# Kernel tuning notes

Measured on AMD Instinct MI355X. Metric: run time of the kernel, lower is better.

The kernel has to match this reference:

```python
import jax, jax.numpy as jnp
import numpy as np

# ---- config (from DAREConfig init_kwargs) ----
TAU = 0.1
RHO_VIS = 0.5          # is_visual=True -> rho_target = rho_vis_target
PREFIX_KAPPA = 64
LAMBDA_RATIO = 1.0
LAMBDA_SOFT = 0.1
LAMBDA_HARD = 1.0

B, S = 256, 32768


def setup_inputs() -> dict:
    key = jax.random.key(0)
    k1, k2 = jax.random.split(key)
    importance = jax.random.normal(k1, (B, S), dtype=jnp.float32)
    modality_mask = jax.random.randint(k2, (B, S), 0, 2) > 0  # bool [B,S]
    return {"importance": importance, "modality_mask": modality_mask}


def reference(importance, modality_mask):
    """Vectorized DAREController.route(is_visual=True, training=True).

    The torch loop over batch with data-dependent k is replaced by a
    per-row k-th-largest threshold: for each row, k_b = min(int(rho*|mm_b|),
    |valid_b|); tokens with score >= k_b-th largest valid score are kept
    (this matches DifferentiableTopK's hard mask soft>0.5, i.e. exactly the
    top-k scores, assuming no ties).
    """
    mm = modality_mask.astype(bool)          # [B,S]
    b, s = importance.shape

    target = jnp.clip(mm.sum(axis=1).astype(jnp.float32) * RHO_VIS, 1.0)  # [B]
    prefix = jnp.arange(s) < min(PREFIX_KAPPA, s)                          # [S]
    eff = mm & ~prefix[None, :]                                            # [B,S] routable tokens
    n_valid = eff.sum(axis=1)                                              # [B]
    k = jnp.minimum(target.astype(jnp.int32), n_valid)                     # [B] per-row top-k size

    neg_inf = jnp.float32(-jnp.inf)
    masked = jnp.where(eff, importance, neg_inf)                           # [B,S]
    sorted_desc = -jnp.sort(-masked, axis=1)                               # [B,S]
    idx = jnp.clip(k - 1, 0, s - 1)                                        # [B]
    thresh = jnp.take_along_axis(sorted_desc, idx[:, None], axis=1)        # [B,1]
    hard = masked >= thresh                                                # top-k of valid tokens

    keep_mask = prefix[None, :] | (hard & (k > 0)[:, None])                # [B,S]

    # ---- training / is_visual losses ----
    kept = (keep_mask & mm).sum(axis=1).astype(jnp.float32)
    denom = mm.sum(axis=1).astype(jnp.float32) + 1e-6
    actual_ratio = kept / denom
    loss_ratio = jnp.mean(jnp.abs(actual_ratio - RHO_VIS))                 # F.l1_loss

    dropped = mm & ~keep_mask
    n_drop = dropped.sum()
    drop_mean = jnp.sum(jnp.where(dropped, importance, 0.0)) / jnp.maximum(n_drop, 1).astype(jnp.float32)
    loss_soft = jnp.where(n_drop > 0, drop_mean, 0.0)

    loss_hard = jnp.mean(jnp.clip(RHO_VIS - actual_ratio, 0.0))

    return (keep_mask,
            LAMBDA_RATIO * loss_ratio,
            LAMBDA_SOFT * loss_soft,
            LAMBDA_HARD * loss_hard)
```

## Files before the change

### kernel.cpp

```cpp
#include <hip/hip_runtime.h>


#define NB 256
#define NS 32768
#define KAPPA 64
#define NT 1024
#define NCPY 64
#define HP 257
#define V4 (NS / NT / 4)

typedef float f32x4 __attribute__((ext_vector_type(4)));
typedef int   i32x4 __attribute__((ext_vector_type(4)));

__device__ __forceinline__ unsigned int fkey(float f) {
    unsigned int u = __float_as_uint(f);
    return (u & 0x80000000u) ? ~u : (u | 0x80000000u);
}

__device__ __forceinline__ float unkey(unsigned int k) {
    unsigned int u = (k & 0x80000000u) ? (k ^ 0x80000000u) : ~k;
    return __uint_as_float(u);
}

__global__ __launch_bounds__(NT) void dare_rows(const float* __restrict__ imp,
                                                const int* __restrict__ mask,
                                                float* __restrict__ keep,
                                                float* __restrict__ stats) {
    __shared__ unsigned int hist0[NCPY * HP];
    __shared__ unsigned int hist[256];
    __shared__ unsigned int wtot[4];
    __shared__ unsigned int sh_mm, sh_eff;
    __shared__ unsigned int sh_pref;
    __shared__ unsigned int sh_rem;
    __shared__ unsigned int sh_kept, sh_ndrop;
    __shared__ float sh_dsum;

    const int row = blockIdx.x;
    const int tid = threadIdx.x;
    const int lane = tid & 63;
    const int wid = tid >> 6;
    const f32x4* rimp4  = (const f32x4*)(imp  + (size_t)row * NS);
    const i32x4* rmask4 = (const i32x4*)(mask + (size_t)row * NS);
    f32x4*       rkeep4 = (f32x4*)      (keep + (size_t)row * NS);

    for (int i = tid; i < NCPY * HP; i += NT) hist0[i] = 0;
    if (tid < 256) hist[tid] = 0;
    if (tid == 0) {
        sh_mm = 0; sh_eff = 0; sh_kept = 0; sh_ndrop = 0; sh_dsum = 0.0f;
        sh_pref = 0; sh_rem = 1;
    }
    __syncthreads();

    unsigned int keys[V4 * 4];
    unsigned int effbits = 0, mmbits = 0;

    #pragma unroll
    for (int i = 0; i < V4; i++) {
        const int idx4 = tid + i * NT;
        const f32x4 v = rimp4[idx4];
        const i32x4 m = rmask4[idx4];
        #pragma unroll
        for (int j = 0; j < 4; j++) {
            const int e = i * 4 + j;
            const int col = idx4 * 4 + j;
            keys[e] = fkey(v[j]);
            const bool mm  = (m[j] != 0);
            const bool eff = mm && (col >= KAPPA);
            mmbits  |= (mm  ? 1u : 0u) << e;
            effbits |= (eff ? 1u : 0u) << e;
        }
    }

    unsigned int* myhist = &hist0[((wid << 2) | (lane & 3)) * HP];
    #pragma unroll
    for (int e = 0; e < V4 * 4; e++) {
        if ((effbits >> e) & 1u) atomicAdd(&myhist[keys[e] >> 24], 1u);
    }

    int mm_local  = __popc(mmbits);
    int eff_local = __popc(effbits);
    #pragma unroll
    for (int off = 32; off; off >>= 1) {
        mm_local  += __shfl_down(mm_local, off);
        eff_local += __shfl_down(eff_local, off);
    }
    if (lane == 0) {
        atomicAdd(&sh_mm,  (unsigned int)mm_local);
        atomicAdd(&sh_eff, (unsigned int)eff_local);
    }
    __syncthreads();

    #pragma unroll
    for (int pass = 0; pass < 4; pass++) {
        const int shift = 24 - 8 * pass;

        if (pass > 0) {
            if (tid < 256) hist[tid] = 0;
            __syncthreads();
            const unsigned int pmask = 0xFFFFFFFFu << (shift + 8);
            const unsigned int pref = sh_pref;
            #pragma unroll
            for (int e = 0; e < V4 * 4; e++) {
                const bool match = ((effbits >> e) & 1u) && ((keys[e] & pmask) == pref);
                if (match) atomicAdd(&hist[(keys[e] >> shift) & 0xFFu], 1u);
            }
            __syncthreads();
        }

        unsigned int h = 0, s = 0;
        if (tid < 256) {
            if (pass == 0) {
                #pragma unroll
                for (int c = 0; c < NCPY; c++) h += hist0[c * HP + tid];
            } else {
                h = hist[tid];
            }
            s = h;
            #pragma unroll
            for (int off = 1; off < 64; off <<= 1) {
                const unsigned int t = __shfl_down(s, off);
                if (lane + off < 64) s += t;
            }
            if (lane == 0) wtot[tid >> 6] = s;
        }
        __syncthreads();
        if (tid < 256) {
            unsigned int sfull = s;
            for (int w = (tid >> 6) + 1; w < 4; w++) sfull += wtot[w];
            unsigned int rem;
            if (pass == 0) {
                const float target = fmaxf((float)sh_mm * 0.5f, 1.0f);
                const int k = min((int)target, (int)sh_eff);
                rem = (unsigned int)max(k, 1);
            } else {
                rem = sh_rem;
            }
            if (sfull >= rem && (sfull - h) < rem) {
                sh_pref = (pass == 0) ? ((unsigned int)tid << 24)
                                      : (sh_pref | ((unsigned int)tid << shift));
                sh_rem = rem - (sfull - h);
            }
        }
        __syncthreads();
    }

    const unsigned int thresh = sh_pref;
    const float targetf = fmaxf((float)sh_mm * 0.5f, 1.0f);
    const bool kpos = (min((int)targetf, (int)sh_eff) > 0);

    int kept_l = 0, ndrop_l = 0;
    float dsum_l = 0.0f;
    #pragma unroll
    for (int i = 0; i < V4; i++) {
        const int idx4 = tid + i * NT;
        f32x4 o;
        #pragma unroll
        for (int j = 0; j < 4; j++) {
            const int e = i * 4 + j;
            const int col = idx4 * 4 + j;
            const bool mm  = (mmbits >> e) & 1u;
            const bool eff = (effbits >> e) & 1u;
            const bool hard = eff && kpos && (keys[e] >= thresh);
            const bool kp = (col < KAPPA) || hard;
            o[j] = kp ? 1.0f : 0.0f;
            kept_l += (kp && mm) ? 1 : 0;
            const bool drop = mm && !kp;
            ndrop_l += drop ? 1 : 0;
            dsum_l += drop ? unkey(keys[e]) : 0.0f;
        }
        rkeep4[idx4] = o;
    }
    #pragma unroll
    for (int off = 32; off; off >>= 1) {
        kept_l  += __shfl_down(kept_l, off);
        ndrop_l += __shfl_down(ndrop_l, off);
        dsum_l  += __shfl_down(dsum_l, off);
    }
    if (lane == 0) {
        atomicAdd(&sh_kept,  (unsigned int)kept_l);
        atomicAdd(&sh_ndrop, (unsigned int)ndrop_l);
        atomicAdd(&sh_dsum,  dsum_l);
    }
    __syncthreads();
    if (tid == 0) {
        stats[row * 4 + 0] = (float)sh_kept;
        stats[row * 4 + 1] = (float)sh_mm;
        stats[row * 4 + 2] = (float)sh_ndrop;
        stats[row * 4 + 3] = sh_dsum;
    }
}

__global__ __launch_bounds__(256) void dare_losses(const float* __restrict__ stats,
                                                   float* __restrict__ out) {
    __shared__ float w_a[4], w_h[4], w_n[4], w_d[4];
    const int tid = threadIdx.x;
    const float kept = stats[tid * 4 + 0];
    const float mmc  = stats[tid * 4 + 1];
    const float nd   = stats[tid * 4 + 2];
    const float ds   = stats[tid * 4 + 3];
    const float ratio = kept / (mmc + 1e-6f);
    float a = fabsf(ratio - 0.5f);
    float h = fmaxf(0.5f - ratio, 0.0f);
    float n = nd, d = ds;
    #pragma unroll
    for (int off = 32; off; off >>= 1) {
        a += __shfl_down(a, off);
        h += __shfl_down(h, off);
        n += __shfl_down(n, off);
        d += __shfl_down(d, off);
    }
    const int wid = tid >> 6, lane = tid & 63;
    if (lane == 0) { w_a[wid] = a; w_h[wid] = h; w_n[wid] = n; w_d[wid] = d; }
    __syncthreads();
    if (tid == 0) {
        float sa = 0.f, shh = 0.f, sn = 0.f, sd = 0.f;
        for (int w = 0; w < 4; w++) { sa += w_a[w]; shh += w_h[w]; sn += w_n[w]; sd += w_d[w]; }
        out[0] = sa / (float)NB;
        out[1] = (sn > 0.0f) ? 0.1f * (sd / fmaxf(sn, 1.0f)) : 0.0f;
        out[2] = shh / (float)NB;
    }
}

extern "C" void kernel_launch(void* const* d_in, const int* in_sizes, int n_in,
                              void* d_out, int out_size, void* d_ws, size_t ws_size,
                              hipStream_t stream) {
    const float* imp  = (const float*)d_in[0];
    const int*   mask = (const int*)d_in[1];
    float* out   = (float*)d_out;
    float* stats = (float*)d_ws;

    dare_rows<<<NB, NT, 0, stream>>>(imp, mask, out, stats);
    dare_losses<<<1, 256, 0, stream>>>(stats, out + (size_t)NB * NS);
}
```

Baseline: 112.4 us.

## Split row kernel into select pass and separate parallel mask-write pass

The single per-row kernel is split in two. A select kernel computes the radix-select threshold and packs the modality mask into a shared bitmap written to workspace. A second kernel launched with 8x more blocks then re-reads importance, applies the threshold, writes the keep mask and accumulates stats with global atomics. The histogram copies are also cut from 64 per block to one per wave. The split is meant to spread the output-write phase across more CUs and shrink shared memory, at the cost of re-reading importance, an extra launch and more bank conflicts in the histogram.

New measurement: 118.9 us. +5.8%, slower.

```diff
diff --git a/kernel.cpp b/kernel.cpp
--- a/kernel.cpp
+++ b/kernel.cpp
@@ -5,35 +5,36 @@
 #define NS 32768
 #define KAPPA 64
 #define NT 1024
-#define NCPY 64
+#define NW (NT / 64)
 #define HP 257
 #define V4 (NS / NT / 4)
 
+#define K2B 256
+#define K2SPLIT 8
+#define K2V4 (NS / K2SPLIT / K2B / 4)
+
 typedef float f32x4 __attribute__((ext_vector_type(4)));
 typedef int   i32x4 __attribute__((ext_vector_type(4)));
+
+#define WS_THRESH (4096 / 4)
+#define WS_KPOS   (5120 / 4)
+#define WS_BM     (8192 / 4)
 
 __device__ __forceinline__ unsigned int fkey(float f) {
     unsigned int u = __float_as_uint(f);
     return (u & 0x80000000u) ? ~u : (u | 0x80000000u);
 }
 
-__device__ __forceinline__ float unkey(unsigned int k) {
-    unsigned int u = (k & 0x80000000u) ? (k ^ 0x80000000u) : ~k;
-    return __uint_as_float(u);
-}
-
-__global__ __launch_bounds__(NT) void dare_rows(const float* __restrict__ imp,
-                                                const int* __restrict__ mask,
-                                                float* __restrict__ keep,
-                                                float* __restrict__ stats) {
-    __shared__ unsigned int hist0[NCPY * HP];
+__global__ __launch_bounds__(NT) void dare_select(const float* __restrict__ imp,
+                                                  const int* __restrict__ mask,
+                                                  unsigned int* __restrict__ ws) {
+    __shared__ unsigned int hist0[NW * HP];
     __shared__ unsigned int hist[256];
+    __shared__ unsigned int bm[NS / 32];
     __shared__ unsigned int wtot[4];
     __shared__ unsigned int sh_mm, sh_eff;
     __shared__ unsigned int sh_pref;
     __shared__ unsigned int sh_rem;
-    __shared__ unsigned int sh_kept, sh_ndrop;
-    __shared__ float sh_dsum;
 
     const int row = blockIdx.x;
     const int tid = threadIdx.x;
@@ -41,14 +42,11 @@
     const int wid = tid >> 6;
     const f32x4* rimp4  = (const f32x4*)(imp  + (size_t)row * NS);
     const i32x4* rmask4 = (const i32x4*)(mask + (size_t)row * NS);
-    f32x4*       rkeep4 = (f32x4*)      (keep + (size_t)row * NS);
-
-    for (int i = tid; i < NCPY * HP; i += NT) hist0[i] = 0;
+
+    for (int i = tid; i < NW * HP; i += NT) hist0[i] = 0;
     if (tid < 256) hist[tid] = 0;
-    if (tid == 0) {
-        sh_mm = 0; sh_eff = 0; sh_kept = 0; sh_ndrop = 0; sh_dsum = 0.0f;
-        sh_pref = 0; sh_rem = 1;
-    }
+    bm[tid] = 0;
+    if (tid == 0) { sh_mm = 0; sh_eff = 0; sh_pref = 0; sh_rem = 1; }
     __syncthreads();
 
     unsigned int keys[V4 * 4];
@@ -71,10 +69,16 @@
         }
     }
 
-    unsigned int* myhist = &hist0[((wid << 2) | (lane & 3)) * HP];
+    unsigned int* myhist = &hist0[wid * HP];
     #pragma unroll
     for (int e = 0; e < V4 * 4; e++) {
         if ((effbits >> e) & 1u) atomicAdd(&myhist[keys[e] >> 24], 1u);
+    }
+    #pragma unroll
+    for (int i = 0; i < V4; i++) {
+        const int idx4 = tid + i * NT;
+        const unsigned int nib = (mmbits >> (i * 4)) & 0xFu;
+        atomicOr(&bm[idx4 >> 3], nib << ((idx4 & 7) * 4));
     }
 
     int mm_local  = __popc(mmbits);
@@ -111,7 +115,7 @@
         if (tid < 256) {
             if (pass == 0) {
                 #pragma unroll
-                for (int c = 0; c < NCPY; c++) h += hist0[c * HP + tid];
+                for (int c = 0; c < NW; c++) h += hist0[c * HP + tid];
             } else {
                 h = hist[tid];
             }
@@ -144,49 +148,78 @@
         __syncthreads();
     }
 
-    const unsigned int thresh = sh_pref;
-    const float targetf = fmaxf((float)sh_mm * 0.5f, 1.0f);
-    const bool kpos = (min((int)targetf, (int)sh_eff) > 0);
+    ws[WS_BM + row * (NS / 32) + tid] = bm[tid];
+    if (tid == 0) {
+        const float target = fmaxf((float)sh_mm * 0.5f, 1.0f);
+        const int k = min((int)target, (int)sh_eff);
+        ws[WS_THRESH + row] = sh_pref;
+        ws[WS_KPOS + row] = (k > 0) ? 1u : 0u;
+        float* stats = (float*)ws;
+        stats[row * 4 + 0] = 0.0f;
+        stats[row * 4 + 1] = (float)sh_mm;
+        stats[row * 4 + 2] = 0.0f;
+        stats[row * 4 + 3] = 0.0f;
+    }
+}
+
+__global__ __launch_bounds__(K2B) void dare_write(const float* __restrict__ imp,
+                                                  const unsigned int* __restrict__ ws,
+                                                  float* __restrict__ keep) {
+    __shared__ float w_k[4], w_n[4], w_d[4];
+
+    const int row = blockIdx.x >> 3;
+    const int q   = blockIdx.x & 7;
+    const int tid = threadIdx.x;
+    const int lane = tid & 63;
+
+    const unsigned int thresh = ws[WS_THRESH + row];
+    const bool kpos = ws[WS_KPOS + row] != 0u;
+    const unsigned int* rbm = ws + WS_BM + row * (NS / 32);
+
+    const f32x4* rimp4  = (const f32x4*)(imp  + (size_t)row * NS);
+    f32x4*       rkeep4 = (f32x4*)      (keep + (size_t)row * NS);
 
     int kept_l = 0, ndrop_l = 0;
     float dsum_l = 0.0f;
-    #pragma unroll
-    for (int i = 0; i < V4; i++) {
-        const int idx4 = tid + i * NT;
+
+    #pragma unroll
+    for (int i = 0; i < K2V4; i++) {
+        const int idx4 = q * (NS / K2SPLIT / 4) + tid + i * K2B;
+        const f32x4 v = rimp4[idx4];
+        const unsigned int nib = (rbm[idx4 >> 3] >> ((idx4 & 7) * 4)) & 0xFu;
         f32x4 o;
         #pragma unroll
         for (int j = 0; j < 4; j++) {
-            const int e = i * 4 + j;
             const int col = idx4 * 4 + j;
-            const bool mm  = (mmbits >> e) & 1u;
-            const bool eff = (effbits >> e) & 1u;
-            const bool hard = eff && kpos && (keys[e] >= thresh);
+            const bool mm  = (nib >> j) & 1u;
+            const bool eff = mm && (col >= KAPPA);
+            const bool hard = eff && kpos && (fkey(v[j]) >= thresh);
             const bool kp = (col < KAPPA) || hard;
             o[j] = kp ? 1.0f : 0.0f;
             kept_l += (kp && mm) ? 1 : 0;
             const bool drop = mm && !kp;
             ndrop_l += drop ? 1 : 0;
-            dsum_l += drop ? unkey(keys[e]) : 0.0f;
+            dsum_l += drop ? v[j] : 0.0f;
         }
         rkeep4[idx4] = o;
     }
+
     #pragma unroll
     for (int off = 32; off; off >>= 1) {
         kept_l  += __shfl_down(kept_l, off);
         ndrop_l += __shfl_down(ndrop_l, off);
         dsum_l  += __shfl_down(dsum_l, off);
     }
-    if (lane == 0) {
-        atomicAdd(&sh_kept,  (unsigned int)kept_l);
-        atomicAdd(&sh_ndrop, (unsigned int)ndrop_l);
-        atomicAdd(&sh_dsum,  dsum_l);
-    }
+    const int wid = tid >> 6;
+    if (lane == 0) { w_k[wid] = (float)kept_l; w_n[wid] = (float)ndrop_l; w_d[wid] = dsum_l; }
     __syncthreads();
     if (tid == 0) {
-        stats[row * 4 + 0] = (float)sh_kept;
-        stats[row * 4 + 1] = (float)sh_mm;
-        stats[row * 4 + 2] = (float)sh_ndrop;
-        stats[row * 4 + 3] = sh_dsum;
+        float sk = 0.f, sn = 0.f, sd = 0.f;
+        for (int w = 0; w < 4; w++) { sk += w_k[w]; sn += w_n[w]; sd += w_d[w]; }
+        float* stats = (float*)ws;
+        atomicAdd(&stats[row * 4 + 0], sk);
+        atomicAdd(&stats[row * 4 + 2], sn);
+        atomicAdd(&stats[row * 4 + 3], sd);
     }
 }
 
@@ -226,9 +259,10 @@
                               hipStream_t stream) {
     const float* imp  = (const float*)d_in[0];
     const int*   mask = (const int*)d_in[1];
-    float* out   = (float*)d_out;
-    float* stats = (float*)d_ws;
-
-    dare_rows<<<NB, NT, 0, stream>>>(imp, mask, out, stats);
-    dare_losses<<<1, 256, 0, stream>>>(stats, out + (size_t)NB * NS);
-}
+    float* out = (float*)d_out;
+    unsigned int* ws = (unsigned int*)d_ws;
+
+    dare_select<<<NB, NT, 0, stream>>>(imp, mask, ws);
+    dare_write<<<NB * K2SPLIT, K2B, 0, stream>>>(imp, ws, out);
+    dare_losses<<<1, 256, 0, stream>>>((const float*)ws, out + (size_t)NB * NS);
+}
```

## Replace 4-pass radix select with 2048-bin histogram plus candidate bitwise select

Applied to the files above, without the earlier changes.

Swaps the four-pass 8-bit radix select for a single 11-bit histogram pass (one shared 2048-bin histogram instead of 64 padded copies). The elements that land in the threshold bin are compacted into shared memory, and one wavefront resolves the remaining 21 bits with ballot-based bitwise selection. Outputs that are clearly above or below the threshold bin are written right away; only vectors containing candidates are deferred until the exact threshold is known. The aim is to cut the three extra full-row histogram passes and their barriers. The cost is more atomic contention on the single histogram, a large shared candidate buffer that lowers occupancy, and a serial 21-bit loop run by only 64 threads.

New measurement: 111.3 us. About the same (-1.0%).

```diff
diff --git a/kernel.cpp b/kernel.cpp
--- a/kernel.cpp
+++ b/kernel.cpp
@@ -5,9 +5,10 @@
 #define NS 32768
 #define KAPPA 64
 #define NT 1024
-#define NCPY 64
-#define HP 257
 #define V4 (NS / NT / 4)
+#define NBIN 2048
+#define NSEG 256
+#define SEGW (NBIN / NSEG)
 
 typedef float f32x4 __attribute__((ext_vector_type(4)));
 typedef int   i32x4 __attribute__((ext_vector_type(4)));
@@ -26,12 +27,11 @@
                                                 const int* __restrict__ mask,
                                                 float* __restrict__ keep,
                                                 float* __restrict__ stats) {
-    __shared__ unsigned int hist0[NCPY * HP];
-    __shared__ unsigned int hist[256];
+    __shared__ unsigned int hist[NBIN];
+    __shared__ unsigned int cand[NS];
     __shared__ unsigned int wtot[4];
-    __shared__ unsigned int sh_mm, sh_eff;
-    __shared__ unsigned int sh_pref;
-    __shared__ unsigned int sh_rem;
+    __shared__ unsigned int sh_mm, sh_eff, sh_cand;
+    __shared__ unsigned int sh_b0, sh_rem, sh_thresh;
     __shared__ unsigned int sh_kept, sh_ndrop;
     __shared__ float sh_dsum;
 
@@ -43,11 +43,12 @@
     const i32x4* rmask4 = (const i32x4*)(mask + (size_t)row * NS);
     f32x4*       rkeep4 = (f32x4*)      (keep + (size_t)row * NS);
 
-    for (int i = tid; i < NCPY * HP; i += NT) hist0[i] = 0;
-    if (tid < 256) hist[tid] = 0;
+    hist[tid] = 0;
+    hist[tid + NT] = 0;
     if (tid == 0) {
-        sh_mm = 0; sh_eff = 0; sh_kept = 0; sh_ndrop = 0; sh_dsum = 0.0f;
-        sh_pref = 0; sh_rem = 1;
+        sh_mm = 0; sh_eff = 0; sh_cand = 0;
+        sh_b0 = 0; sh_rem = 1; sh_thresh = 0;
+        sh_kept = 0; sh_ndrop = 0; sh_dsum = 0.0f;
     }
     __syncthreads();
 
@@ -71,10 +72,9 @@
         }
     }
 
-    unsigned int* myhist = &hist0[((wid << 2) | (lane & 3)) * HP];
     #pragma unroll
     for (int e = 0; e < V4 * 4; e++) {
-        if ((effbits >> e) & 1u) atomicAdd(&myhist[keys[e] >> 24], 1u);
+        if ((effbits >> e) & 1u) atomicAdd(&hist[keys[e] >> 21], 1u);
     }
 
     int mm_local  = __popc(mmbits);
@@ -90,86 +90,142 @@
     }
     __syncthreads();
 
-    #pragma unroll
-    for (int pass = 0; pass < 4; pass++) {
-        const int shift = 24 - 8 * pass;
-
-        if (pass > 0) {
-            if (tid < 256) hist[tid] = 0;
-            __syncthreads();
-            const unsigned int pmask = 0xFFFFFFFFu << (shift + 8);
-            const unsigned int pref = sh_pref;
-            #pragma unroll
-            for (int e = 0; e < V4 * 4; e++) {
-                const bool match = ((effbits >> e) & 1u) && ((keys[e] & pmask) == pref);
-                if (match) atomicAdd(&hist[(keys[e] >> shift) & 0xFFu], 1u);
-            }
-            __syncthreads();
-        }
-
-        unsigned int h = 0, s = 0;
-        if (tid < 256) {
-            if (pass == 0) {
-                #pragma unroll
-                for (int c = 0; c < NCPY; c++) h += hist0[c * HP + tid];
-            } else {
-                h = hist[tid];
-            }
-            s = h;
-            #pragma unroll
-            for (int off = 1; off < 64; off <<= 1) {
-                const unsigned int t = __shfl_down(s, off);
-                if (lane + off < 64) s += t;
-            }
-            if (lane == 0) wtot[tid >> 6] = s;
-        }
-        __syncthreads();
-        if (tid < 256) {
-            unsigned int sfull = s;
-            for (int w = (tid >> 6) + 1; w < 4; w++) sfull += wtot[w];
-            unsigned int rem;
-            if (pass == 0) {
-                const float target = fmaxf((float)sh_mm * 0.5f, 1.0f);
-                const int k = min((int)target, (int)sh_eff);
-                rem = (unsigned int)max(k, 1);
-            } else {
-                rem = sh_rem;
-            }
-            if (sfull >= rem && (sfull - h) < rem) {
-                sh_pref = (pass == 0) ? ((unsigned int)tid << 24)
-                                      : (sh_pref | ((unsigned int)tid << shift));
-                sh_rem = rem - (sfull - h);
-            }
-        }
-        __syncthreads();
-    }
-
-    const unsigned int thresh = sh_pref;
-    const float targetf = fmaxf((float)sh_mm * 0.5f, 1.0f);
-    const bool kpos = (min((int)targetf, (int)sh_eff) > 0);
+    unsigned int r[SEGW];
+    unsigned int hsum = 0, s = 0;
+    if (tid < NSEG) {
+        #pragma unroll
+        for (int b = 0; b < SEGW; b++) { r[b] = hist[tid * SEGW + b]; hsum += r[b]; }
+        s = hsum;
+        #pragma unroll
+        for (int off = 1; off < 64; off <<= 1) {
+            const unsigned int t = __shfl_down(s, off);
+            if (lane + off < 64) s += t;
+        }
+        if (lane == 0) wtot[tid >> 6] = s;
+    }
+    __syncthreads();
+    if (tid < NSEG) {
+        unsigned int sfull = s;
+        for (int w = (tid >> 6) + 1; w < 4; w++) sfull += wtot[w];
+        const float target = fmaxf((float)sh_mm * 0.5f, 1.0f);
+        const int k = min((int)target, (int)sh_eff);
+        const unsigned int rem = (unsigned int)max(k, 1);
+        const unsigned int above = sfull - hsum;
+        if (sfull >= rem && above < rem) {
+            unsigned int cum = above;
+            #pragma unroll
+            for (int b = SEGW - 1; b >= 0; b--) {
+                if (cum + r[b] >= rem) { sh_b0 = tid * SEGW + b; sh_rem = rem - cum; break; }
+                cum += r[b];
+            }
+        }
+    }
+    __syncthreads();
+
+    const unsigned int b0 = sh_b0;
+    const bool kpos = (sh_eff > 0);
 
     int kept_l = 0, ndrop_l = 0;
     float dsum_l = 0.0f;
+    unsigned int defer = 0;
+
     #pragma unroll
     for (int i = 0; i < V4; i++) {
         const int idx4 = tid + i * NT;
-        f32x4 o;
+        unsigned int cm = 0;
         #pragma unroll
         for (int j = 0; j < 4; j++) {
             const int e = i * 4 + j;
-            const int col = idx4 * 4 + j;
-            const bool mm  = (mmbits >> e) & 1u;
             const bool eff = (effbits >> e) & 1u;
-            const bool hard = eff && kpos && (keys[e] >= thresh);
-            const bool kp = (col < KAPPA) || hard;
-            o[j] = kp ? 1.0f : 0.0f;
-            kept_l += (kp && mm) ? 1 : 0;
-            const bool drop = mm && !kp;
-            ndrop_l += drop ? 1 : 0;
-            dsum_l += drop ? unkey(keys[e]) : 0.0f;
-        }
-        rkeep4[idx4] = o;
-    }
+            const bool is_cand = kpos && eff && ((keys[e] >> 21) == b0);
+            cm |= (is_cand ? 1u : 0u) << j;
+        }
+        if (cm) {
+            defer |= 1u << i;
+            #pragma unroll
+            for (int j = 0; j < 4; j++) {
+                if ((cm >> j) & 1u) {
+                    const unsigned int pos = atomicAdd(&sh_cand, 1u);
+                    cand[pos] = keys[i * 4 + j];
+                }
+            }
+        } else {
+            f32x4 o;
+            #pragma unroll
+            for (int j = 0; j < 4; j++) {
+                const int e = i * 4 + j;
+                const int col = idx4 * 4 + j;
+                const bool mm  = (mmbits >> e) & 1u;
+                const bool eff = (effbits >> e) & 1u;
+                const bool hard = kpos && eff && ((keys[e] >> 21) > b0);
+                const bool kp = (col < KAPPA) || hard;
+                o[j] = kp ? 1.0f : 0.0f;
+                kept_l += (kp && mm) ? 1 : 0;
+                const bool drop = mm && !kp;
+                ndrop_l += drop ? 1 : 0;
+                dsum_l += drop ? unkey(keys[e]) : 0.0f;
+            }
+            rkeep4[idx4] = o;
+        }
+    }
+    __syncthreads();
+
+    if (tid < 64) {
+        const unsigned int cnt = sh_cand;
+        if (cnt > 0) {
+            unsigned int rem = sh_rem;
+            unsigned int pref = 0;
+            const int slots = (int)((cnt + 63u) >> 6);
+            unsigned int lowreg[16];
+            #pragma unroll
+            for (int sl = 0; sl < 16; sl++) {
+                const unsigned int idx = (unsigned int)lane + ((unsigned int)sl << 6);
+                lowreg[sl] = (idx < cnt) ? (cand[idx] & 0x1FFFFFu) : 0xFFFFFFFFu;
+            }
+            for (int bit = 20; bit >= 0; bit--) {
+                const unsigned int hi = pref >> (bit + 1);
+                unsigned int cnt1 = 0;
+                for (int sl = 0; sl < slots; sl++) {
+                    unsigned int lw;
+                    if (sl < 16) lw = lowreg[sl];
+                    else {
+                        const unsigned int idx = (unsigned int)lane + ((unsigned int)sl << 6);
+                        lw = (idx < cnt) ? (cand[idx] & 0x1FFFFFu) : 0xFFFFFFFFu;
+                    }
+                    const bool m = (lw >> (bit + 1)) == hi && ((lw >> bit) & 1u);
+                    cnt1 += (unsigned int)__popcll(__ballot(m));
+                }
+                if (cnt1 >= rem) pref |= 1u << bit; else rem -= cnt1;
+            }
+            if (lane == 0) sh_thresh = (b0 << 21) | pref;
+        }
+    }
+    __syncthreads();
+
+    const unsigned int thresh = sh_thresh;
+    #pragma unroll
+    for (int i = 0; i < V4; i++) {
+        if ((defer >> i) & 1u) {
+            const int idx4 = tid + i * NT;
+            f32x4 o;
+            #pragma unroll
+            for (int j = 0; j < 4; j++) {
+                const int e = i * 4 + j;
+                const int col = idx4 * 4 + j;
+                const bool mm  = (mmbits >> e) & 1u;
+                const bool eff = (effbits >> e) & 1u;
+                const bool hard = kpos && eff && (keys[e] >= thresh);
+                const bool kp = (col < KAPPA) || hard;
+                o[j] = kp ? 1.0f : 0.0f;
+                kept_l += (kp && mm) ? 1 : 0;
+                const bool drop = mm && !kp;
+                ndrop_l += drop ? 1 : 0;
+                dsum_l += drop ? unkey(keys[e]) : 0.0f;
+            }
+            rkeep4[idx4] = o;
+        }
+    }
+
     #pragma unroll
     for (int off = 32; off; off >>= 1) {
         kept_l  += __shfl_down(kept_l, off);
```

## Stage importance row in LDS via direct global-to-LDS loads, single shared histogram

Applied to the files above, without the earlier changes.

The importance row is now loaded straight into a 128KB LDS buffer with global_load_lds and re-read from LDS in every radix pass, so keys no longer sit in registers. The 64 privatized first-pass histogram copies are dropped in favour of one shared 256-bin histogram, and the mm/eff counts use per-wave slots instead of atomics. This cuts register pressure and histogram init/merge work, at the cost of repeated LDS reads and more atomic contention on the single histogram. The 128KB LDS footprint also limits residency to one block per CU.

Result: slower. 118.8 us (+5.7%).

```diff
diff --git a/kernel.cpp b/kernel.cpp
--- a/kernel.cpp
+++ b/kernel.cpp
@@ -5,34 +5,28 @@
 #define NS 32768
 #define KAPPA 64
 #define NT 1024
-#define NCPY 64
-#define HP 257
+#define NW (NT / 64)
 #define V4 (NS / NT / 4)
 
 typedef float f32x4 __attribute__((ext_vector_type(4)));
 typedef int   i32x4 __attribute__((ext_vector_type(4)));
-
-__device__ __forceinline__ unsigned int fkey(float f) {
-    unsigned int u = __float_as_uint(f);
+typedef unsigned int u32;
+
+__device__ __forceinline__ u32 fkey(float f) {
+    u32 u = __float_as_uint(f);
     return (u & 0x80000000u) ? ~u : (u | 0x80000000u);
-}
-
-__device__ __forceinline__ float unkey(unsigned int k) {
-    unsigned int u = (k & 0x80000000u) ? (k ^ 0x80000000u) : ~k;
-    return __uint_as_float(u);
 }
 
 __global__ __launch_bounds__(NT) void dare_rows(const float* __restrict__ imp,
                                                 const int* __restrict__ mask,
                                                 float* __restrict__ keep,
                                                 float* __restrict__ stats) {
-    __shared__ unsigned int hist0[NCPY * HP];
-    __shared__ unsigned int hist[256];
-    __shared__ unsigned int wtot[4];
-    __shared__ unsigned int sh_mm, sh_eff;
-    __shared__ unsigned int sh_pref;
-    __shared__ unsigned int sh_rem;
-    __shared__ unsigned int sh_kept, sh_ndrop;
+    __shared__ float simp[NS];
+    __shared__ u32 hist[256];
+    __shared__ u32 wtot[4];
+    __shared__ u32 wred_mm[NW], wred_eff[NW];
+    __shared__ u32 sh_mm, sh_eff, sh_pref, sh_rem;
+    __shared__ u32 sh_kept, sh_ndrop;
     __shared__ float sh_dsum;
 
     const int row = blockIdx.x;
@@ -43,40 +37,36 @@
     const i32x4* rmask4 = (const i32x4*)(mask + (size_t)row * NS);
     f32x4*       rkeep4 = (f32x4*)      (keep + (size_t)row * NS);
 
-    for (int i = tid; i < NCPY * HP; i += NT) hist0[i] = 0;
     if (tid < 256) hist[tid] = 0;
-    if (tid == 0) {
-        sh_mm = 0; sh_eff = 0; sh_kept = 0; sh_ndrop = 0; sh_dsum = 0.0f;
-        sh_pref = 0; sh_rem = 1;
-    }
-    __syncthreads();
-
-    unsigned int keys[V4 * 4];
-    unsigned int effbits = 0, mmbits = 0;
-
-    #pragma unroll
-    for (int i = 0; i < V4; i++) {
-        const int idx4 = tid + i * NT;
-        const f32x4 v = rimp4[idx4];
-        const i32x4 m = rmask4[idx4];
+    if (tid == 0) { sh_pref = 0; sh_rem = 1; sh_kept = 0; sh_ndrop = 0; sh_dsum = 0.0f; }
+
+    #pragma unroll
+    for (int i = 0; i < V4; i++) {
+        const int idx4 = tid + i * NT;
+        __builtin_amdgcn_global_load_lds(
+            (const __attribute__((address_space(1))) u32*)(&rimp4[idx4]),
+            (__attribute__((address_space(3))) u32*)(&simp[idx4 * 4]),
+            16, 0, 0);
+    }
+
+    i32x4 mv[V4];
+    #pragma unroll
+    for (int i = 0; i < V4; i++) mv[i] = rmask4[tid + i * NT];
+
+    u32 mmbits = 0, effbits = 0;
+    #pragma unroll
+    for (int i = 0; i < V4; i++) {
+        const int idx4 = tid + i * NT;
         #pragma unroll
         for (int j = 0; j < 4; j++) {
             const int e = i * 4 + j;
             const int col = idx4 * 4 + j;
-            keys[e] = fkey(v[j]);
-            const bool mm  = (m[j] != 0);
+            const bool mm  = (mv[i][j] != 0);
             const bool eff = mm && (col >= KAPPA);
             mmbits  |= (mm  ? 1u : 0u) << e;
             effbits |= (eff ? 1u : 0u) << e;
         }
     }
-
-    unsigned int* myhist = &hist0[((wid << 2) | (lane & 3)) * HP];
-    #pragma unroll
-    for (int e = 0; e < V4 * 4; e++) {
-        if ((effbits >> e) & 1u) atomicAdd(&myhist[keys[e] >> 24], 1u);
-    }
-
     int mm_local  = __popc(mmbits);
     int eff_local = __popc(effbits);
     #pragma unroll
@@ -84,9 +74,24 @@
         mm_local  += __shfl_down(mm_local, off);
         eff_local += __shfl_down(eff_local, off);
     }
-    if (lane == 0) {
-        atomicAdd(&sh_mm,  (unsigned int)mm_local);
-        atomicAdd(&sh_eff, (unsigned int)eff_local);
+    if (lane == 0) { wred_mm[wid] = (u32)mm_local; wred_eff[wid] = (u32)eff_local; }
+
+    __syncthreads();
+
+    #pragma unroll
+    for (int i = 0; i < V4; i++) {
+        const int idx4 = tid + i * NT;
+        const f32x4 v = *(const f32x4*)&simp[idx4 * 4];
+        #pragma unroll
+        for (int j = 0; j < 4; j++) {
+            if ((effbits >> (i * 4 + j)) & 1u) atomicAdd(&hist[fkey(v[j]) >> 24], 1u);
+        }
+    }
+    if (tid == 0) {
+        u32 sm = 0, se = 0;
+        #pragma unroll
+        for (int w = 0; w < NW; w++) { sm += wred_mm[w]; se += wred_eff[w]; }
+        sh_mm = sm; sh_eff = se;
     }
     __syncthreads();
 
@@ -97,62 +102,62 @@
         if (pass > 0) {
             if (tid < 256) hist[tid] = 0;
             __syncthreads();
-            const unsigned int pmask = 0xFFFFFFFFu << (shift + 8);
-            const unsigned int pref = sh_pref;
+            const u32 pmask = 0xFFFFFFFFu << (shift + 8);
+            const u32 pref = sh_pref;
             #pragma unroll
-            for (int e = 0; e < V4 * 4; e++) {
-                const bool match = ((effbits >> e) & 1u) && ((keys[e] & pmask) == pref);
-                if (match) atomicAdd(&hist[(keys[e] >> shift) & 0xFFu], 1u);
+            for (int i = 0; i < V4; i++) {
+                const int idx4 = tid + i * NT;
+                const f32x4 v = *(const f32x4*)&simp[idx4 * 4];
+                #pragma unroll
+                for (int j = 0; j < 4; j++) {
+                    const u32 key = fkey(v[j]);
+                    const bool match = ((effbits >> (i * 4 + j)) & 1u) && ((key & pmask) == pref);
+                    if (match) atomicAdd(&hist[(key >> shift) & 0xFFu], 1u);
+                }
             }
             __syncthreads();
         }
 
-        unsigned int h = 0, s = 0;
+        u32 h = 0, s = 0;
         if (tid < 256) {
-            if (pass == 0) {
-                #pragma unroll
-                for (int c = 0; c < NCPY; c++) h += hist0[c * HP + tid];
-            } else {
-                h = hist[tid];
-            }
+            h = hist[tid];
             s = h;
             #pragma unroll
             for (int off = 1; off < 64; off <<= 1) {
-                const unsigned int t = __shfl_down(s, off);
+                const u32 t = __shfl_down(s, off);
                 if (lane + off < 64) s += t;
             }
             if (lane == 0) wtot[tid >> 6] = s;
         }
         __syncthreads();
         if (tid < 256) {
-            unsigned int sfull = s;
+            u32 sfull = s;
             for (int w = (tid >> 6) + 1; w < 4; w++) sfull += wtot[w];
-            unsigned int rem;
+            u32 rem;
             if (pass == 0) {
                 const float target = fmaxf((float)sh_mm * 0.5f, 1.0f);
                 const int k = min((int)target, (int)sh_eff);
-                rem = (unsigned int)max(k, 1);
+                rem = (u32)max(k, 1);
             } else {
                 rem = sh_rem;
             }
             if (sfull >= rem && (sfull - h) < rem) {
-                sh_pref = (pass == 0) ? ((unsigned int)tid << 24)
-                                      : (sh_pref | ((unsigned int)tid << shift));
+                sh_pref = (pass == 0) ? ((u32)tid << 24) : (sh_pref | ((u32)tid << shift));
                 sh_rem = rem - (sfull - h);
             }
         }
         __syncthreads();
     }
 
-    const unsigned int thresh = sh_pref;
-    const float targetf = fmaxf((float)sh_mm * 0.5f, 1.0f);
-    const bool kpos = (min((int)targetf, (int)sh_eff) > 0);
+    const u32 thresh = sh_pref;
+    const bool kpos = (sh_eff > 0);
 
     int kept_l = 0, ndrop_l = 0;
     float dsum_l = 0.0f;
     #pragma unroll
     for (int i = 0; i < V4; i++) {
         const int idx4 = tid + i * NT;
+        const f32x4 v = *(const f32x4*)&simp[idx4 * 4];
         f32x4 o;
         #pragma unroll
         for (int j = 0; j < 4; j++) {
@@ -160,13 +165,13 @@
             const int col = idx4 * 4 + j;
             const bool mm  = (mmbits >> e) & 1u;
             const bool eff = (effbits >> e) & 1u;
-            const bool hard = eff && kpos && (keys[e] >= thresh);
+            const bool hard = kpos && eff && (fkey(v[j]) >= thresh);
             const bool kp = (col < KAPPA) || hard;
             o[j] = kp ? 1.0f : 0.0f;
             kept_l += (kp && mm) ? 1 : 0;
             const bool drop = mm && !kp;
             ndrop_l += drop ? 1 : 0;
-            dsum_l += drop ? unkey(keys[e]) : 0.0f;
+            dsum_l += drop ? v[j] : 0.0f;
         }
         rkeep4[idx4] = o;
     }
@@ -177,8 +182,8 @@
         dsum_l  += __shfl_down(dsum_l, off);
     }
     if (lane == 0) {
-        atomicAdd(&sh_kept,  (unsigned int)kept_l);
-        atomicAdd(&sh_ndrop, (unsigned int)ndrop_l);
+        atomicAdd(&sh_kept,  (u32)kept_l);
+        atomicAdd(&sh_ndrop, (u32)ndrop_l);
         atomicAdd(&sh_dsum,  dsum_l);
     }
     __syncthreads();
```
